# Kernel optimization log

Hardware: AMD Instinct MI355X
Metric: run time of the kernel (lower is better)

## Reference

```python
import jax, jax.numpy as jnp
import numpy as np

BETA = 0.25  # commitment cost (init kwarg)


def setup_inputs() -> dict:
    key = jax.random.key(0)
    k1, k2 = jax.random.split(key)
    B, C, H, W = 8, 256, 64, 64
    K = 8192  # codebook_size
    z = jax.random.normal(k1, (B, C, H, W), dtype=jnp.float32)
    # torch init is uniform(-1/K, 1/K); use same scale
    codebook = jax.random.uniform(k2, (K, C), dtype=jnp.float32,
                                  minval=-1.0 / K, maxval=1.0 / K)
    return {"z": z, "codebook": codebook}


def reference(z, codebook):
    # z: [B, C, H, W] -> [B, H, W, C]
    z_bhwc = jnp.transpose(z, (0, 2, 3, 1))
    D = codebook.shape[1]
    zf = z_bhwc.reshape(-1, D)  # [N, D]
    # squared euclidean distances: ||z||^2 + ||e||^2 - 2 z.e  -> [N, K]
    d = (jnp.sum(zf * zf, axis=1, keepdims=True)
         + jnp.sum(codebook * codebook, axis=1)
         - 2.0 * jnp.einsum('nd,kd->nk', zf, codebook))
    min_encoding_indices = jnp.argmin(d, axis=1)  # [N]
    z_q = codebook[min_encoding_indices].reshape(z_bhwc.shape)  # [B,H,W,C]
    sg = jax.lax.stop_gradient
    # legacy=False branch
    loss = (BETA * jnp.mean((sg(z_q) - z_bhwc) ** 2)
            + jnp.mean((z_q - sg(z_bhwc)) ** 2))
    # straight-through estimator
    z_q = z_bhwc + sg(z_q - z_bhwc)
    z_q = jnp.transpose(z_q, (0, 3, 1, 2))  # back to [B, C, H, W]
    return z_q, loss, min_encoding_indices
```

## Files before the change

kernel.cpp:

```cpp
#include <hip/hip_runtime.h>
#include <hip/hip_bf16.h>
#include <math.h>

typedef unsigned short u16;
typedef unsigned int u32;
typedef unsigned long long u64;
typedef __attribute__((ext_vector_type(8))) _Float16 f16x8;
typedef __attribute__((ext_vector_type(4))) float f32x4;

#define B_   8
#define C_   256
#define HW_  4096
#define N_   32768
#define K_   8192

#define O_LOSSP 0ULL
#define O_E2    16384ULL
#define O_ZN2   49152ULL
#define O_IDX   180224ULL
#define O_ZT    311296ULL
#define O_AP    33865728ULL
#define O_BP    50642944ULL
#define O_CAND  54837248ULL
#define WS_NEED 88391680ULL

#define THRESH_T 9e-5f

#define GSWZ(r) (((r) >> 1) & 3)

__device__ __forceinline__ u16 f2h(float f) {
    _Float16 h = (_Float16)f;
    return __builtin_bit_cast(u16, h);
}

__device__ __forceinline__ void gload16(const void* g, void* l) {
    __builtin_amdgcn_global_load_lds((const __attribute__((address_space(1))) void*)g,
                                     (__attribute__((address_space(3))) void*)l, 16, 0, 0);
}


__global__ __launch_bounds__(256) void vq_prep(const float* __restrict__ z,
                                               const float* __restrict__ cb,
                                               float* __restrict__ zT,
                                               u16* __restrict__ Ap,
                                               u16* __restrict__ Bp,
                                               float* __restrict__ zn2g,
                                               float* __restrict__ e2g) {
    __shared__ float zl[128][65];
    const int tid = threadIdx.x;

    if (blockIdx.x < 128) {
        const int k0 = blockIdx.x * 64;
        const int r = tid >> 2;
        const int u4 = tid & 3;
        const int k = k0 + r;
        const int r7 = k & 127;
        double eacc = 0.0;
        #pragma unroll
        for (int kc8 = 0; kc8 < 8; ++kc8) {
            const float* src = cb + (size_t)k * C_ + kc8 * 32 + u4 * 8;
            float4 v0 = *(const float4*)(src);
            float4 v1 = *(const float4*)(src + 4);
            float vals[8] = { v0.x, v0.y, v0.z, v0.w, v1.x, v1.y, v1.z, v1.w };
            u16 tmp[8];
            #pragma unroll
            for (int j = 0; j < 8; ++j) {
                eacc += (double)vals[j] * (double)vals[j];
                tmp[j] = f2h(vals[j] * 8192.0f);
            }
            char* dst = (char*)Bp + ((size_t)((k >> 7) * 8 + kc8)) * 8192
                      + r7 * 64 + ((u4 * 16) ^ (GSWZ(r7) << 4));
            *(uint4*)dst = *(uint4*)tmp;
        }
        eacc += __shfl_xor(eacc, 1);
        eacc += __shfl_xor(eacc, 2);
        if (u4 == 0) e2g[k] = (float)eacc;
        return;
    }

    const int bidz = blockIdx.x - 128;
    const int bb = bidz >> 6;
    const int hwc = bidz & 63;
    const int hw0 = hwc * 64;
    const int n0 = bb * HW_ + hw0;
    const int lane = tid & 63, wid = tid >> 6;
    const int r = tid >> 2;
    const int u4 = tid & 3;
    const int n = n0 + r;
    const int r7 = n & 127;
    double zacc = 0.0;

    for (int h = 0; h < 2; ++h) {
        __syncthreads();
        for (int c0 = 0; c0 < 128; c0 += 4) {
            int c = c0 + (tid >> 6);
            zl[c][tid & 63] = z[((size_t)(bb * C_ + h * 128 + c)) * HW_ + hw0 + (tid & 63)];
        }
        __syncthreads();
        for (int it = 0; it < 8; ++it) {
            int rp = it * 8 + wid * 2 + (lane >> 5);
            int c4 = (lane & 31) * 4;
            float4 v = { zl[c4][rp], zl[c4 + 1][rp], zl[c4 + 2][rp], zl[c4 + 3][rp] };
            *(float4*)(zT + (size_t)(n0 + rp) * C_ + h * 128 + c4) = v;
        }
        #pragma unroll
        for (int q = 0; q < 4; ++q) {
            u16 tmp[8];
            #pragma unroll
            for (int j = 0; j < 8; ++j) {
                float f = zl[q * 32 + u4 * 8 + j][r];
                zacc += (double)f * (double)f;
                tmp[j] = f2h(f);
            }
            char* dst = (char*)Ap + ((size_t)((n >> 7) * 8 + h * 4 + q)) * 8192
                      + r7 * 64 + ((u4 * 16) ^ (GSWZ(r7) << 4));
            *(uint4*)dst = *(uint4*)tmp;
        }
    }
    zacc += __shfl_xor(zacc, 1);
    zacc += __shfl_xor(zacc, 2);
    if (u4 == 0) zn2g[n] = (float)zacc;
}

__global__ __launch_bounds__(256) void vq_gemm_top2(const u16* __restrict__ Ap,
                                                    const u16* __restrict__ Bp,
                                                    u32* __restrict__ cand) {
    __shared__ char lds[32768];
    const int tid = threadIdx.x;
    const int lane = tid & 63, wid = tid >> 6;
    const int wm = wid >> 1, wn = wid & 1;
    const int l15 = lane & 15, l4 = lane >> 4;

    const int raw = blockIdx.x;
    const int m_tile = raw >> 6;
    const int n_tile = (raw & 7) * 8 + ((raw >> 3) & 7);

    f32x4 acc[4][4];
    #pragma unroll
    for (int i = 0; i < 4; ++i)
        #pragma unroll
        for (int j = 0; j < 4; ++j) acc[i][j] = (f32x4){0.f, 0.f, 0.f, 0.f};

    int rc[4], rz[4], xc[4], xz[4];
    #pragma unroll
    for (int f = 0; f < 4; ++f) {
        rc[f] = wm * 64 + f * 16 + l15;
        rz[f] = wn * 64 + f * 16 + l15;
        xc[f] = GSWZ(rc[f]) << 4;
        xz[f] = GSWZ(rz[f]) << 4;
    }
    const int ob = l4 * 16;

    const char* codes_src = (const char*)Bp + (size_t)n_tile * 65536;
    const char* z_src     = (const char*)Ap + (size_t)m_tile * 65536;

    #define STAGE(buf, kc)                                                        \
        do {                                                                      \
            const char* cs_ = codes_src + (size_t)(kc) * 8192;                    \
            const char* zs_ = z_src + (size_t)(kc) * 8192;                        \
            char* lb_ = lds + (buf) * 16384;                                      \
            gload16(cs_ + tid * 16, lb_ + tid * 16);                              \
            gload16(cs_ + 4096 + tid * 16, lb_ + 4096 + tid * 16);                \
            gload16(zs_ + tid * 16, lb_ + 8192 + tid * 16);                       \
            gload16(zs_ + 4096 + tid * 16, lb_ + 12288 + tid * 16);               \
        } while (0)

    #define COMPUTE(buf)                                                          \
        do {                                                                      \
            const char* base_ = lds + (buf) * 16384;                              \
            f16x8 la[4], lb[4];                                                   \
            _Pragma("unroll")                                                     \
            for (int f = 0; f < 4; ++f) {                                         \
                la[f] = *(const f16x8*)(base_ + rc[f] * 64 + (ob ^ xc[f]));       \
                lb[f] = *(const f16x8*)(base_ + 8192 + rz[f] * 64 + (ob ^ xz[f]));\
            }                                                                     \
            _Pragma("unroll")                                                     \
            for (int fm = 0; fm < 4; ++fm)                                        \
                _Pragma("unroll")                                                 \
                for (int fn = 0; fn < 4; ++fn)                                    \
                    acc[fm][fn] = __builtin_amdgcn_mfma_f32_16x16x32_f16(         \
                        la[fm], lb[fn], acc[fm][fn], 0, 0, 0);                    \
        } while (0)

    #define FENCE() __builtin_amdgcn_sched_barrier(0)

    STAGE(0, 0);
    STAGE(1, 1);
    #pragma unroll
    for (int kc = 0; kc < 8; ++kc) {
        if (kc < 7) { asm volatile("s_waitcnt vmcnt(4)" ::: "memory"); }
        else        { asm volatile("s_waitcnt vmcnt(0)" ::: "memory"); }
        FENCE();
        __builtin_amdgcn_s_barrier();
        FENCE();
        COMPUTE(kc & 1);
        if (kc < 6) {
            asm volatile("s_waitcnt lgkmcnt(0)" ::: "memory");
            FENCE();
            __builtin_amdgcn_s_barrier();
            FENCE();
            STAGE(kc & 1, kc + 2);
        }
    }

    #undef STAGE
    #undef COMPUTE
    #undef FENCE

    const int ktile = n_tile * 2 + wm;
    #pragma unroll
    for (int fn = 0; fn < 4; ++fn) {
        u32 m1 = 0xFFFFFFFFu, m2 = 0xFFFFFFFFu;
        #pragma unroll
        for (int fm = 0; fm < 4; ++fm) {
            #pragma unroll
            for (int rv = 0; rv < 4; ++rv) {
                float w = fmaf(acc[fm][fn][rv], -0x1p-12f, 0.5f);
                u32 p = (__float_as_uint(w) & ~63u) | (u32)(fm * 16 + l4 * 4 + rv);
                u32 t = m1 > p ? m1 : p;
                m1 = m1 < p ? m1 : p;
                m2 = m2 < t ? m2 : t;
            }
        }
        #pragma unroll
        for (int off = 16; off <= 32; off <<= 1) {
            u32 b1 = __shfl_xor(m1, off);
            u32 b2 = __shfl_xor(m2, off);
            u32 t = m1 > b1 ? m1 : b1;
            m1 = m1 < b1 ? m1 : b1;
            u32 s2 = m2 < b2 ? m2 : b2;
            m2 = s2 < t ? s2 : t;
        }
        if (l4 == 0) {
            int rowg = m_tile * 128 + wn * 64 + fn * 16 + l15;
            *(uint2*)(cand + (size_t)rowg * 256 + ktile * 2) = make_uint2(m1, m2);
        }
    }
}

__global__ __launch_bounds__(256) void vq_pick(const u32* __restrict__ cand,
                                               const float* __restrict__ zT,
                                               const float* __restrict__ cb,
                                               const float* __restrict__ e2g,
                                               const float* __restrict__ zn2g,
                                               int* __restrict__ idxg,
                                               float* __restrict__ out) {
    const int lane = threadIdx.x & 63, wid = threadIdx.x >> 6;
    const int row = blockIdx.x * 4 + wid;
    const uint4 e = ((const uint4*)(cand + (size_t)row * 256))[lane];
    u32 m = e.x < e.y ? e.x : e.y;
    u32 mzw = e.z < e.w ? e.z : e.w;
    m = m < mzw ? m : mzw;
    #pragma unroll
    for (int off = 32; off >= 1; off >>= 1) {
        u32 o = __shfl_xor(m, off);
        m = o < m ? o : m;
    }
    const float thr = __uint_as_float(m & ~63u) + THRESH_T;
    const u32 ev[4] = { e.x, e.y, e.z, e.w };
    u64 msk[4];
    int tot = 0;
    #pragma unroll
    for (int j = 0; j < 4; ++j) {
        msk[j] = __ballot(__uint_as_float(ev[j] & ~63u) <= thr);
        tot += __popcll((unsigned long long)msk[j]);
    }
    int bk;
    if (tot == 1) {
        const int j = msk[0] ? 0 : (msk[1] ? 1 : (msk[2] ? 2 : 3));
        const int l = __ffsll((unsigned long long)msk[j]) - 1;
        const u32 val = __shfl(ev[j], l);
        bk = ((l * 4 + j) >> 1) * 64 + (int)(val & 63u);
    } else {
        const float4 zv = *(const float4*)(zT + (size_t)row * C_ + lane * 4);
        const float zn2a = zn2g[row];
        float bd = INFINITY;
        bk = 0x7fffffff;
        #pragma unroll
        for (int j = 0; j < 4; ++j) {
            u64 mj = msk[j];
            while (mj) {
                const int l = __ffsll((unsigned long long)mj) - 1;
                mj &= mj - 1;
                const u32 val = __shfl(ev[j], l);
                const int k = ((l * 4 + j) >> 1) * 64 + (int)(val & 63u);
                const float4 cv = *(const float4*)(cb + (size_t)k * C_ + lane * 4);
                double s = (double)zv.x * cv.x + (double)zv.y * cv.y
                         + (double)zv.z * cv.z + (double)zv.w * cv.w;
                #pragma unroll
                for (int off = 32; off >= 1; off >>= 1) s += __shfl_xor(s, off);
                const float sf = (float)s;
                const float d = (zn2a + e2g[k]) - 2.0f * sf;
                if (d < bd || (d == bd && k < bk)) { bd = d; bk = k; }
            }
        }
    }
    if (lane == 0) {
        idxg[row] = bk;
        out[8388609 + row] = (float)bk;
    }
}

__global__ __launch_bounds__(256) void vq_zq_loss_kernel(const float* __restrict__ z,
                                                         const float* __restrict__ cb,
                                                         const int* __restrict__ idxg,
                                                         float* __restrict__ out,
                                                         double* __restrict__ partial) {
    double acc = 0.0;
    for (size_t i4 = (size_t)blockIdx.x * 256 + threadIdx.x; i4 < 2097152ULL;
         i4 += 2048ULL * 256ULL) {
        const size_t i = i4 * 4;
        const int hw = (int)(i & 4095);
        const int bc = (int)(i >> 12);
        const int c = bc & 255;
        const int b = bc >> 8;
        const int n = (b << 12) + hw;
        const float4 zv = *(const float4*)(z + i);
        const int k0 = idxg[n], k1 = idxg[n + 1], k2 = idxg[n + 2], k3 = idxg[n + 3];
        const float t0 = cb[(size_t)k0 * C_ + c] - zv.x;
        const float t1 = cb[(size_t)k1 * C_ + c] - zv.y;
        const float t2 = cb[(size_t)k2 * C_ + c] - zv.z;
        const float t3 = cb[(size_t)k3 * C_ + c] - zv.w;
        float4 o = { zv.x + t0, zv.y + t1, zv.z + t2, zv.w + t3 };
        *(float4*)(out + i) = o;
        acc += (double)t0 * t0 + (double)t1 * t1 + (double)t2 * t2 + (double)t3 * t3;
    }
    #pragma unroll
    for (int off = 32; off >= 1; off >>= 1) acc += __shfl_xor(acc, off);
    __shared__ double ls[4];
    const int lane = threadIdx.x & 63, wid = threadIdx.x >> 6;
    if (lane == 0) ls[wid] = acc;
    __syncthreads();
    if (threadIdx.x == 0) partial[blockIdx.x] = ls[0] + ls[1] + ls[2] + ls[3];
}

__global__ __launch_bounds__(256) void vq_loss_final(const double* __restrict__ partial,
                                                     float* __restrict__ out) {
    double acc = 0.0;
    for (int j = threadIdx.x; j < 2048; j += 256) acc += partial[j];
    #pragma unroll
    for (int off = 32; off >= 1; off >>= 1) acc += __shfl_xor(acc, off);
    __shared__ double ls[4];
    const int lane = threadIdx.x & 63, wid = threadIdx.x >> 6;
    if (lane == 0) ls[wid] = acc;
    __syncthreads();
    if (threadIdx.x == 0)
        out[8388608] = (float)(1.25 * (ls[0] + ls[1] + ls[2] + ls[3]) / 8388608.0);
}

__global__ __launch_bounds__(256) void vq_e2_old(const float* __restrict__ cb,
                                                 float* __restrict__ e2g) {
    int lane = threadIdx.x & 63;
    int w = threadIdx.x >> 6;
    int k = blockIdx.x * 4 + w;
    const float4 v = *reinterpret_cast<const float4*>(cb + (size_t)k * C_ + lane * 4);
    double acc = (double)v.x * v.x + (double)v.y * v.y
               + (double)v.z * v.z + (double)v.w * v.w;
    #pragma unroll
    for (int off = 32; off >= 1; off >>= 1) acc += __shfl_xor(acc, off);
    if (lane == 0) e2g[k] = (float)acc;
}

__global__ __launch_bounds__(256) void vq_zn2_old(const float* __restrict__ z,
                                                  float* __restrict__ zn2g) {
    int n = blockIdx.x * 256 + threadIdx.x;
    int b = n >> 12;
    int hw = n & 4095;
    const float* p = z + (size_t)b * C_ * HW_ + hw;
    double acc = 0.0;
    #pragma unroll 8
    for (int c = 0; c < C_; ++c) {
        float v = p[(size_t)c * HW_];
        acc += (double)v * (double)v;
    }
    zn2g[n] = (float)acc;
}

__global__ __launch_bounds__(256) void vq_argmin_old(const float* __restrict__ z,
                                                     const float* __restrict__ cb,
                                                     const float* __restrict__ e2g,
                                                     const float* __restrict__ zn2g,
                                                     int* __restrict__ idxg) {
    __shared__ float zt[C_][32];
    __shared__ float et[64][64];
    const int tid = threadIdx.x;
    const int n0 = blockIdx.x * 32;
    const int b = n0 >> 12;
    const int hw0 = n0 & 4095;
    {
        const int nn = tid & 31;
        const int c8 = tid >> 5;
        #pragma unroll
        for (int j = 0; j < 32; ++j) {
            const int c = j * 8 + c8;
            zt[c][nn] = z[(size_t)(b * C_ + c) * HW_ + hw0 + nn];
        }
    }
    const int cg = tid & 15;
    const int rg = tid >> 4;
    const int r0 = rg * 2;
    __syncthreads();
    const float zn2a = zn2g[n0 + r0];
    const float zn2b = zn2g[n0 + r0 + 1];
    float dmin0 = INFINITY, dmin1 = INFINITY;
    int imin0 = 0, imin1 = 0;
    const int kk = tid >> 2;
    const int c4 = (tid & 3) * 16;
    for (int kt = 0; kt < K_; kt += 64) {
        double s00 = 0, s01 = 0, s02 = 0, s03 = 0;
        double s10 = 0, s11 = 0, s12 = 0, s13 = 0;
        for (int cc = 0; cc < C_; cc += 64) {
            __syncthreads();
            {
                const float* src = cb + (size_t)(kt + kk) * C_ + cc + c4;
                #pragma unroll
                for (int j = 0; j < 16; j += 4) {
                    const float4 v = *reinterpret_cast<const float4*>(src + j);
                    et[c4 + j + 0][kk] = v.x;
                    et[c4 + j + 1][kk] = v.y;
                    et[c4 + j + 2][kk] = v.z;
                    et[c4 + j + 3][kk] = v.w;
                }
            }
            __syncthreads();
            #pragma unroll 4
            for (int c2 = 0; c2 < 64; ++c2) {
                const float2 zv = *reinterpret_cast<const float2*>(&zt[cc + c2][r0]);
                const float4 ev = *reinterpret_cast<const float4*>(&et[c2][cg * 4]);
                const double z0 = (double)zv.x, z1 = (double)zv.y;
                s00 += z0 * ev.x; s01 += z0 * ev.y; s02 += z0 * ev.z; s03 += z0 * ev.w;
                s10 += z1 * ev.x; s11 += z1 * ev.y; s12 += z1 * ev.z; s13 += z1 * ev.w;
            }
        }
        const int kbase = kt + cg * 4;
        const float sf0[4] = {(float)s00, (float)s01, (float)s02, (float)s03};
        const float sf1[4] = {(float)s10, (float)s11, (float)s12, (float)s13};
        #pragma unroll
        for (int j = 0; j < 4; ++j) {
            const int k = kbase + j;
            const float e2k = e2g[k];
            const float d0 = (zn2a + e2k) - 2.0f * sf0[j];
            const float d1 = (zn2b + e2k) - 2.0f * sf1[j];
            if (d0 < dmin0) { dmin0 = d0; imin0 = k; }
            if (d1 < dmin1) { dmin1 = d1; imin1 = k; }
        }
    }
    #pragma unroll
    for (int off = 8; off >= 1; off >>= 1) {
        const float od0 = __shfl_xor(dmin0, off);
        const int   oi0 = __shfl_xor(imin0, off);
        const float od1 = __shfl_xor(dmin1, off);
        const int   oi1 = __shfl_xor(imin1, off);
        if (od0 < dmin0 || (od0 == dmin0 && oi0 < imin0)) { dmin0 = od0; imin0 = oi0; }
        if (od1 < dmin1 || (od1 == dmin1 && oi1 < imin1)) { dmin1 = od1; imin1 = oi1; }
    }
    if (cg == 0) {
        idxg[n0 + r0]     = imin0;
        idxg[n0 + r0 + 1] = imin1;
    }
}

__global__ __launch_bounds__(256) void vq_final_old(const int* __restrict__ idxg,
                                                    float* __restrict__ out) {
    const int i = blockIdx.x * 256 + threadIdx.x;
    out[8388609 + i] = (float)idxg[i];
}

extern "C" void kernel_launch(void* const* d_in, const int* in_sizes, int n_in,
                              void* d_out, int out_size, void* d_ws, size_t ws_size,
                              hipStream_t stream) {
    const float* z  = (const float*)d_in[0];
    const float* cb = (const float*)d_in[1];
    float* out = (float*)d_out;
    char* ws = (char*)d_ws;

    double* lossp = (double*)(ws + O_LOSSP);
    float*  e2g  = (float*)(ws + O_E2);
    float*  zn2g = (float*)(ws + O_ZN2);
    int*    idxg = (int*)(ws + O_IDX);

    if (ws_size >= WS_NEED) {
        float* zT   = (float*)(ws + O_ZT);
        u16*   Ap   = (u16*)(ws + O_AP);
        u16*   Bp   = (u16*)(ws + O_BP);
        u32*   cand = (u32*)(ws + O_CAND);

        hipLaunchKernelGGL(vq_prep, dim3(640), dim3(256), 0, stream,
                           z, cb, zT, Ap, Bp, zn2g, e2g);
        hipLaunchKernelGGL(vq_gemm_top2, dim3(16384), dim3(256), 0, stream, Ap, Bp, cand);
        hipLaunchKernelGGL(vq_pick, dim3(N_ / 4), dim3(256), 0, stream,
                           cand, zT, cb, e2g, zn2g, idxg, out);
    } else {
        hipLaunchKernelGGL(vq_e2_old, dim3(K_ / 4), dim3(256), 0, stream, cb, e2g);
        hipLaunchKernelGGL(vq_zn2_old, dim3(N_ / 256), dim3(256), 0, stream, z, zn2g);
        hipLaunchKernelGGL(vq_argmin_old, dim3(N_ / 32), dim3(256), 0, stream,
                           z, cb, e2g, zn2g, idxg);
        hipLaunchKernelGGL(vq_final_old, dim3(N_ / 256), dim3(256), 0, stream, idxg, out);
    }

    hipLaunchKernelGGL(vq_zq_loss_kernel, dim3(2048), dim3(256), 0, stream,
                       z, cb, idxg, out, lossp);
    hipLaunchKernelGGL(vq_loss_final, dim3(1), dim3(256), 0, stream, lossp, out);
}
```

Before: 223.8 us.

## Switch codebook GEMM to 32x32x16 MFMA and simplify LDS double-buffer pipeline

Result: slower. 242.2 us (+8.2%).

```diff
diff --git a/kernel.cpp b/kernel.cpp
--- a/kernel.cpp
+++ b/kernel.cpp
@@ -7,6 +7,7 @@
 typedef unsigned long long u64;
 typedef __attribute__((ext_vector_type(8))) _Float16 f16x8;
 typedef __attribute__((ext_vector_type(4))) float f32x4;
+typedef __attribute__((ext_vector_type(16))) float f32x16;
 
 #define B_   8
 #define C_   256
@@ -129,27 +130,29 @@
     const int tid = threadIdx.x;
     const int lane = tid & 63, wid = tid >> 6;
     const int wm = wid >> 1, wn = wid & 1;
-    const int l15 = lane & 15, l4 = lane >> 4;
+    const int l31 = lane & 31, lhi = lane >> 5;
 
     const int raw = blockIdx.x;
     const int m_tile = raw >> 6;
     const int n_tile = (raw & 7) * 8 + ((raw >> 3) & 7);
 
-    f32x4 acc[4][4];
-    #pragma unroll
-    for (int i = 0; i < 4; ++i)
-        #pragma unroll
-        for (int j = 0; j < 4; ++j) acc[i][j] = (f32x4){0.f, 0.f, 0.f, 0.f};
-
-    int rc[4], rz[4], xc[4], xz[4];
-    #pragma unroll
-    for (int f = 0; f < 4; ++f) {
-        rc[f] = wm * 64 + f * 16 + l15;
-        rz[f] = wn * 64 + f * 16 + l15;
-        xc[f] = GSWZ(rc[f]) << 4;
-        xz[f] = GSWZ(rz[f]) << 4;
-    }
-    const int ob = l4 * 16;
+    f32x16 acc[2][2];
+    #pragma unroll
+    for (int i = 0; i < 2; ++i)
+        #pragma unroll
+        for (int j = 0; j < 2; ++j)
+            acc[i][j] = (f32x16)(0.0f);
+
+    int rcv[2], xcv[2], rzv[2], xzv[2];
+    #pragma unroll
+    for (int f = 0; f < 2; ++f) {
+        rcv[f] = wm * 64 + f * 32 + l31;
+        xcv[f] = GSWZ(rcv[f]) << 4;
+        rzv[f] = wn * 64 + f * 32 + l31;
+        xzv[f] = GSWZ(rzv[f]) << 4;
+    }
+    const int gof0 = lhi * 16;
+    const int gof1 = 32 + lhi * 16;
 
     const char* codes_src = (const char*)Bp + (size_t)n_tile * 65536;
     const char* z_src     = (const char*)Ap + (size_t)m_tile * 65536;
@@ -165,74 +168,67 @@
             gload16(zs_ + 4096 + tid * 16, lb_ + 12288 + tid * 16);               \
         } while (0)
 
+    #define KSTEP(base_, gof_)                                                    \
+        do {                                                                      \
+            f16x8 la[2], lb[2];                                                   \
+            _Pragma("unroll")                                                     \
+            for (int f = 0; f < 2; ++f)                                           \
+                la[f] = *(const f16x8*)((base_) + rcv[f] * 64 + ((gof_) ^ xcv[f]));\
+            _Pragma("unroll")                                                     \
+            for (int f = 0; f < 2; ++f)                                           \
+                lb[f] = *(const f16x8*)((base_) + 8192 + rzv[f] * 64               \
+                                        + ((gof_) ^ xzv[f]));                     \
+            _Pragma("unroll")                                                     \
+            for (int cf = 0; cf < 2; ++cf)                                        \
+                _Pragma("unroll")                                                 \
+                for (int rf = 0; rf < 2; ++rf)                                    \
+                    acc[cf][rf] = __builtin_amdgcn_mfma_f32_32x32x16_f16(         \
+                        la[cf], lb[rf], acc[cf][rf], 0, 0, 0);                    \
+        } while (0)
+
     #define COMPUTE(buf)                                                          \
         do {                                                                      \
             const char* base_ = lds + (buf) * 16384;                              \
-            f16x8 la[4], lb[4];                                                   \
-            _Pragma("unroll")                                                     \
-            for (int f = 0; f < 4; ++f) {                                         \
-                la[f] = *(const f16x8*)(base_ + rc[f] * 64 + (ob ^ xc[f]));       \
-                lb[f] = *(const f16x8*)(base_ + 8192 + rz[f] * 64 + (ob ^ xz[f]));\
-            }                                                                     \
-            _Pragma("unroll")                                                     \
-            for (int fm = 0; fm < 4; ++fm)                                        \
-                _Pragma("unroll")                                                 \
-                for (int fn = 0; fn < 4; ++fn)                                    \
-                    acc[fm][fn] = __builtin_amdgcn_mfma_f32_16x16x32_f16(         \
-                        la[fm], lb[fn], acc[fm][fn], 0, 0, 0);                    \
+            KSTEP(base_, gof0);                                                   \
+            KSTEP(base_, gof1);                                                   \
         } while (0)
 
-    #define FENCE() __builtin_amdgcn_sched_barrier(0)
-
     STAGE(0, 0);
-    STAGE(1, 1);
     #pragma unroll
     for (int kc = 0; kc < 8; ++kc) {
-        if (kc < 7) { asm volatile("s_waitcnt vmcnt(4)" ::: "memory"); }
-        else        { asm volatile("s_waitcnt vmcnt(0)" ::: "memory"); }
-        FENCE();
-        __builtin_amdgcn_s_barrier();
-        FENCE();
+        __syncthreads();
+        if (kc < 7) STAGE((kc + 1) & 1, kc + 1);
         COMPUTE(kc & 1);
-        if (kc < 6) {
-            asm volatile("s_waitcnt lgkmcnt(0)" ::: "memory");
-            FENCE();
-            __builtin_amdgcn_s_barrier();
-            FENCE();
-            STAGE(kc & 1, kc + 2);
-        }
     }
 
     #undef STAGE
+    #undef KSTEP
     #undef COMPUTE
-    #undef FENCE
 
     const int ktile = n_tile * 2 + wm;
     #pragma unroll
-    for (int fn = 0; fn < 4; ++fn) {
+    for (int rf = 0; rf < 2; ++rf) {
         u32 m1 = 0xFFFFFFFFu, m2 = 0xFFFFFFFFu;
         #pragma unroll
-        for (int fm = 0; fm < 4; ++fm) {
+        for (int cf = 0; cf < 2; ++cf) {
             #pragma unroll
-            for (int rv = 0; rv < 4; ++rv) {
-                float w = fmaf(acc[fm][fn][rv], -0x1p-12f, 0.5f);
-                u32 p = (__float_as_uint(w) & ~63u) | (u32)(fm * 16 + l4 * 4 + rv);
+            for (int rg = 0; rg < 16; ++rg) {
+                float w = fmaf(acc[cf][rf][rg], -0x1p-12f, 0.5f);
+                u32 code6 = (u32)(cf * 32 + (rg & 3) + 8 * (rg >> 2) + 4 * lhi);
+                u32 p = (__float_as_uint(w) & ~63u) | code6;
                 u32 t = m1 > p ? m1 : p;
                 m1 = m1 < p ? m1 : p;
                 m2 = m2 < t ? m2 : t;
             }
         }
-        #pragma unroll
-        for (int off = 16; off <= 32; off <<= 1) {
-            u32 b1 = __shfl_xor(m1, off);
-            u32 b2 = __shfl_xor(m2, off);
-            u32 t = m1 > b1 ? m1 : b1;
-            m1 = m1 < b1 ? m1 : b1;
-            u32 s2 = m2 < b2 ? m2 : b2;
-            m2 = s2 < t ? s2 : t;
-        }
-        if (l4 == 0) {
-            int rowg = m_tile * 128 + wn * 64 + fn * 16 + l15;
+        u32 b1 = __shfl_xor(m1, 32);
+        u32 b2 = __shfl_xor(m2, 32);
+        u32 t = m1 > b1 ? m1 : b1;
+        m1 = m1 < b1 ? m1 : b1;
+        u32 s2 = m2 < b2 ? m2 : b2;
+        m2 = s2 < t ? s2 : t;
+        if (lane < 32) {
+            int rowg = m_tile * 128 + wn * 64 + rf * 32 + lane;
             *(uint2*)(cand + (size_t)rowg * 256 + ktile * 2) = make_uint2(m1, m2);
         }
     }
```
